# Kernel tuning notes

Measured on AMD Instinct MI355X. Metric: run time of the kernel, lower is better.

The kernel has to match this reference:

```python
import jax, jax.numpy as jnp
import numpy as np

N_NODES = 100000
N_EDGES = 1600000
NODE_F = 8   # augmented node features
EDGE_F = 2   # augmented edge features
GLOB_F = 1
HID = 16
L = 3        # message passing steps

EDGE_IN = GLOB_F + EDGE_F + 2 * NODE_F   # 19
NODE_IN = GLOB_F + EDGE_F + NODE_F       # 11
GLOB_IN = EDGE_F + NODE_F + GLOB_F       # 11


def setup_inputs() -> dict:
    key = jax.random.key(0)
    ks = jax.random.split(key, 20)
    inp = {
        "x": jax.random.normal(ks[0], (N_NODES, NODE_F), dtype=jnp.float32),
        "edge_index": jax.random.randint(ks[1], (2, N_EDGES), 0, N_NODES, dtype=jnp.int32),
        "edge_attr": jax.random.normal(ks[2], (N_EDGES, EDGE_F), dtype=jnp.float32),
        "g": jax.random.normal(ks[3], (1, GLOB_F), dtype=jnp.float32),
    }
    s = 0.1
    inp["edge_W1"] = jax.random.normal(ks[4], (L, EDGE_IN, HID), dtype=jnp.float32) * s
    inp["edge_b1"] = jnp.zeros((L, HID), dtype=jnp.float32)
    inp["edge_W2"] = jax.random.normal(ks[5], (L, HID, EDGE_F), dtype=jnp.float32) * s
    inp["edge_b2"] = jnp.zeros((L, EDGE_F), dtype=jnp.float32)
    inp["node_W1"] = jax.random.normal(ks[6], (L, NODE_IN, HID), dtype=jnp.float32) * s
    inp["node_b1"] = jnp.zeros((L, HID), dtype=jnp.float32)
    inp["node_W2"] = jax.random.normal(ks[7], (L, HID, NODE_F), dtype=jnp.float32) * s
    inp["node_b2"] = jnp.zeros((L, NODE_F), dtype=jnp.float32)
    inp["glob_W1"] = jax.random.normal(ks[8], (L, GLOB_IN, HID), dtype=jnp.float32) * s
    inp["glob_b1"] = jnp.zeros((L, HID), dtype=jnp.float32)
    inp["glob_W2"] = jax.random.normal(ks[9], (L, HID, GLOB_F), dtype=jnp.float32) * s
    inp["glob_b2"] = jnp.zeros((L, GLOB_F), dtype=jnp.float32)
    return inp


def _mlp(h, W1, b1, W2, b2):
    # two-layer MLP with ReLU after first layer only (activate_final=False, no layer_norm)
    return jnp.maximum(h @ W1 + b1, 0.0) @ W2 + b2


def reference(x, edge_index, edge_attr, g,
              edge_W1, edge_b1, edge_W2, edge_b2,
              node_W1, node_b1, node_W2, node_b2,
              glob_W1, glob_b1, glob_W2, glob_b2):
    row, col = edge_index[0], edge_index[1]
    n = x.shape[0]
    for l in range(L):
        g_e = jnp.broadcast_to(g, (row.shape[0], GLOB_F))
        # edge block: gather node features along edges, concat, MLP -> [E, EDGE_F]
        e_in = jnp.concatenate([g_e, x[row], x[col], edge_attr], axis=1)
        edge_emb = _mlp(e_in, edge_W1[l], edge_b1[l], edge_W2[l], edge_b2[l])
        # sum-aggregate edge embeddings to source nodes
        agg = jax.ops.segment_sum(edge_emb, row, num_segments=n)
        g_n = jnp.broadcast_to(g, (n, GLOB_F))
        node_emb = _mlp(jnp.concatenate([g_n, x, agg], axis=1),
                        node_W1[l], node_b1[l], node_W2[l], node_b2[l])
        # global block on mean-aggregated edge/node embeddings
        edge_gl = jnp.mean(edge_emb, axis=0, keepdims=True)
        node_gl = jnp.mean(node_emb, axis=0, keepdims=True)
        g = _mlp(jnp.concatenate([node_gl, edge_gl, g], axis=1),
                 glob_W1[l], glob_b1[l], glob_W2[l], glob_b2[l])
        x, edge_attr = node_emb, edge_emb
    return x  # final node embeddings [N, NODE_F]
```

## Files before the change

### kernel.cpp

```cpp
#include <hip/hip_runtime.h>

#define NN 100000
#define NE 1600000
#define CH 4096
#define NCHUNK ((NE + CH - 1) / CH)
#define NBUCK ((NN + 255) / 256)

__device__ __forceinline__ float wave_red(float v) {
#pragma unroll
    for (int off = 32; off > 0; off >>= 1) v += __shfl_down(v, off, 64);
    return v;
}

__global__ __launch_bounds__(256) void hist_kernel(
    const int* __restrict__ ei, int* __restrict__ hist)
{
    __shared__ int h[NBUCK];
    int t = threadIdx.x, c = blockIdx.x;
    for (int b = t; b < NBUCK; b += 256) h[b] = 0;
    __syncthreads();
    int base = c * CH;
    for (int i = t; i < CH; i += 256) {
        int e = base + i;
        if (e < NE) atomicAdd(&h[ei[e] >> 8], 1);
    }
    __syncthreads();
    for (int b = t; b < NBUCK; b += 256) hist[c * NBUCK + b] = h[b];
}

__global__ __launch_bounds__(512) void bscan_kernel(
    const int* __restrict__ hist, int* __restrict__ baseT, int* __restrict__ colTotal)
{
    __shared__ int buf[2][512];
    int b = blockIdx.x, t = threadIdx.x;
    int v = (t < NCHUNK) ? hist[t * NBUCK + b] : 0;
    buf[0][t] = v;
    __syncthreads();
    int src = 0;
    for (int d = 1; d < 512; d <<= 1) {
        int nv = buf[src][t] + ((t >= d) ? buf[src][t - d] : 0);
        buf[src ^ 1][t] = nv;
        src ^= 1;
        __syncthreads();
    }
    if (t < NCHUNK) baseT[b * NCHUNK + t] = buf[src][t] - v;
    if (t == NCHUNK - 1) colTotal[b] = buf[src][t];
}

__global__ __launch_bounds__(512) void boff_kernel(
    const int* __restrict__ colTotal, int* __restrict__ b_off)
{
    __shared__ int buf[2][512];
    int t = threadIdx.x;
    int v = (t < NBUCK) ? colTotal[t] : 0;
    buf[0][t] = v;
    __syncthreads();
    int src = 0;
    for (int d = 1; d < 512; d <<= 1) {
        int nv = buf[src][t] + ((t >= d) ? buf[src][t - d] : 0);
        buf[src ^ 1][t] = nv;
        src ^= 1;
        __syncthreads();
    }
    if (t < NBUCK) b_off[t] = buf[src][t] - v;
    if (t == NBUCK - 1) b_off[NBUCK] = buf[src][t];
}

__global__ __launch_bounds__(256) void fillb_kernel(
    const int* __restrict__ ei, const float* __restrict__ eattr,
    const int* __restrict__ baseT, const int* __restrict__ b_off,
    float4* __restrict__ rec)
{
    __shared__ int sslot[NBUCK];
    int t = threadIdx.x, c = blockIdx.x;
    for (int b = t; b < NBUCK; b += 256)
        sslot[b] = b_off[b] + baseT[b * NCHUNK + c];
    __syncthreads();
    int base = c * CH;
    for (int i = t; i < CH; i += 256) {
        int e = base + i;
        if (e < NE) {
            int row = ei[e];
            int slot = atomicAdd(&sslot[row >> 8], 1);
            float2 ea = reinterpret_cast<const float2*>(eattr)[e];
            float4 v;
            v.x = __int_as_float(row);
            v.y = __int_as_float(ei[NE + e]);
            v.z = ea.x; v.w = ea.y;
            rec[slot] = v;
        }
    }
}

__global__ __launch_bounds__(256) void prep_kernel(
    const float* __restrict__ x, const float* __restrict__ W1,
    float* __restrict__ Pr, float* __restrict__ Pc)
{
    int i = blockIdx.x * 256 + threadIdx.x;
    if (i >= NN) return;
    const float4* xi = reinterpret_cast<const float4*>(x + (size_t)i * 8);
    float4 a0 = xi[0], a1 = xi[1];
    float xv[8] = {a0.x, a0.y, a0.z, a0.w, a1.x, a1.y, a1.z, a1.w};
    float pr[16], pc[16];
#pragma unroll
    for (int q = 0; q < 16; q++) { pr[q] = 0.f; pc[q] = 0.f; }
#pragma unroll
    for (int k = 0; k < 8; k++) {
        float v = xv[k];
#pragma unroll
        for (int q = 0; q < 16; q++) {
            pr[q] += v * W1[(1 + k) * 16 + q];
            pc[q] += v * W1[(9 + k) * 16 + q];
        }
    }
    float4* po = reinterpret_cast<float4*>(Pr + (size_t)i * 16);
#pragma unroll
    for (int t = 0; t < 4; t++)
        po[t] = make_float4(pr[4 * t], pr[4 * t + 1], pr[4 * t + 2], pr[4 * t + 3]);
    float4* qo = reinterpret_cast<float4*>(Pc + (size_t)i * 16);
#pragma unroll
    for (int t = 0; t < 4; t++)
        qo[t] = make_float4(pc[4 * t], pc[4 * t + 1], pc[4 * t + 2], pc[4 * t + 3]);
}

template <bool WRITE_REC, bool NEED_SUM, bool HAS_NEXT>
__global__ __launch_bounds__(256, 4) void fused_kernel(
    float4* __restrict__ rec, const int* __restrict__ b_off,
    const float* __restrict__ PrIn, const float* __restrict__ PcIn,
    const float* __restrict__ gptr,
    const float* __restrict__ eW1, const float* __restrict__ eB1,
    const float* __restrict__ eW2, const float* __restrict__ eB2,
    const float* __restrict__ x,
    const float* __restrict__ nW1, const float* __restrict__ nB1,
    const float* __restrict__ nW2, const float* __restrict__ nB2,
    const float* __restrict__ nextW1,
    float* __restrict__ PrOut, float* __restrict__ PcOut,
    float* __restrict__ xout, float* __restrict__ sums)
{
    __shared__ float sPrT[16 * 256];
    __shared__ float sagg[256][2];
    __shared__ float redE[4][2];
    __shared__ float redN[4][8];
    int tid = threadIdx.x;
    sagg[tid][0] = 0.f; sagg[tid][1] = 0.f;

    int n0 = blockIdx.x * 256;
    int nrow = n0 + tid;
    if (nrow < NN) {
        const float4* ps = reinterpret_cast<const float4*>(PrIn + (size_t)nrow * 16);
        float4 p0 = ps[0], p1 = ps[1], p2 = ps[2], p3 = ps[3];
        sPrT[0 * 256 + tid]  = p0.x; sPrT[1 * 256 + tid]  = p0.y;
        sPrT[2 * 256 + tid]  = p0.z; sPrT[3 * 256 + tid]  = p0.w;
        sPrT[4 * 256 + tid]  = p1.x; sPrT[5 * 256 + tid]  = p1.y;
        sPrT[6 * 256 + tid]  = p1.z; sPrT[7 * 256 + tid]  = p1.w;
        sPrT[8 * 256 + tid]  = p2.x; sPrT[9 * 256 + tid]  = p2.y;
        sPrT[10 * 256 + tid] = p2.z; sPrT[11 * 256 + tid] = p2.w;
        sPrT[12 * 256 + tid] = p3.x; sPrT[13 * 256 + tid] = p3.y;
        sPrT[14 * 256 + tid] = p3.z; sPrT[15 * 256 + tid] = p3.w;
    }
    __syncthreads();

    int e0 = b_off[blockIdx.x], e1 = b_off[blockIdx.x + 1];

    float gval = gptr[0];
    float gterm[16];
#pragma unroll
    for (int q = 0; q < 16; q++) gterm[q] = eB1[q] + gval * eW1[q];

    float t0 = 0.f, t1 = 0.f;
    for (int e = e0 + tid; e < e1; e += 256) {
        float4 r = rec[e];
        int row = __float_as_int(r.x);
        int col = __float_as_int(r.y);
        float ea0 = r.z, ea1 = r.w;
        int li = row - n0;
        const float4* pc = reinterpret_cast<const float4*>(PcIn + (size_t)col * 16);
        float4 c0 = pc[0], c1 = pc[1], c2 = pc[2], c3 = pc[3];
        float h[16];
#pragma unroll
        for (int q = 0; q < 16; q++) h[q] = gterm[q] + sPrT[q * 256 + li];
        h[0]  += c0.x; h[1]  += c0.y; h[2]  += c0.z; h[3]  += c0.w;
        h[4]  += c1.x; h[5]  += c1.y; h[6]  += c1.z; h[7]  += c1.w;
        h[8]  += c2.x; h[9]  += c2.y; h[10] += c2.z; h[11] += c2.w;
        h[12] += c3.x; h[13] += c3.y; h[14] += c3.z; h[15] += c3.w;
#pragma unroll
        for (int q = 0; q < 16; q++) {
            h[q] += ea0 * eW1[17 * 16 + q];
            h[q] += ea1 * eW1[18 * 16 + q];
        }
        float s0 = eB2[0], s1 = eB2[1];
#pragma unroll
        for (int q = 0; q < 16; q++) {
            float rr = fmaxf(h[q], 0.f);
            s0 += rr * eW2[2 * q];
            s1 += rr * eW2[2 * q + 1];
        }
        if (WRITE_REC) {
            float4 w;
            w.x = r.x; w.y = r.y; w.z = s0; w.w = s1;
            rec[e] = w;
        }
        atomicAdd(&sagg[li][0], s0);
        atomicAdd(&sagg[li][1], s1);
        t0 += s0; t1 += s1;
    }

    if (NEED_SUM) {
        float r0 = wave_red(t0);
        float r1 = wave_red(t1);
        int wave = tid >> 6, lane = tid & 63;
        if (lane == 0) { redE[wave][0] = r0; redE[wave][1] = r1; }
    }
    __syncthreads();
    if (NEED_SUM && tid == 0) {
        atomicAdd(&sums[0], redE[0][0] + redE[1][0] + redE[2][0] + redE[3][0]);
        atomicAdd(&sums[1], redE[0][1] + redE[1][1] + redE[2][1] + redE[3][1]);
    }

    int n = n0 + tid;
    float out[8];
#pragma unroll
    for (int m = 0; m < 8; m++) out[m] = 0.f;

    if (n < NN) {
        float in[11];
        in[0] = gval;
        const float4* xi = reinterpret_cast<const float4*>(x + (size_t)n * 8);
        float4 a0 = xi[0], a1 = xi[1];
        in[1] = a0.x; in[2] = a0.y; in[3] = a0.z; in[4] = a0.w;
        in[5] = a1.x; in[6] = a1.y; in[7] = a1.z; in[8] = a1.w;
        in[9] = sagg[tid][0]; in[10] = sagg[tid][1];

        float h[16];
#pragma unroll
        for (int q = 0; q < 16; q++) h[q] = nB1[q];
#pragma unroll
        for (int k = 0; k < 11; k++) {
            float v = in[k];
#pragma unroll
            for (int q = 0; q < 16; q++) h[q] += v * nW1[k * 16 + q];
        }
#pragma unroll
        for (int m = 0; m < 8; m++) out[m] = nB2[m];
#pragma unroll
        for (int q = 0; q < 16; q++) {
            float hq = fmaxf(h[q], 0.f);
#pragma unroll
            for (int m = 0; m < 8; m++) out[m] += hq * nW2[q * 8 + m];
        }
        float4* xo = reinterpret_cast<float4*>(xout + (size_t)n * 8);
        xo[0] = make_float4(out[0], out[1], out[2], out[3]);
        xo[1] = make_float4(out[4], out[5], out[6], out[7]);

        if (HAS_NEXT) {
            float pr[16], pc[16];
#pragma unroll
            for (int q = 0; q < 16; q++) { pr[q] = 0.f; pc[q] = 0.f; }
#pragma unroll
            for (int k = 0; k < 8; k++) {
                float v = out[k];
#pragma unroll
                for (int q = 0; q < 16; q++) {
                    pr[q] += v * nextW1[(1 + k) * 16 + q];
                    pc[q] += v * nextW1[(9 + k) * 16 + q];
                }
            }
            float4* po = reinterpret_cast<float4*>(PrOut + (size_t)n * 16);
#pragma unroll
            for (int t = 0; t < 4; t++)
                po[t] = make_float4(pr[4*t], pr[4*t+1], pr[4*t+2], pr[4*t+3]);
            float4* qo = reinterpret_cast<float4*>(PcOut + (size_t)n * 16);
#pragma unroll
            for (int t = 0; t < 4; t++)
                qo[t] = make_float4(pc[4*t], pc[4*t+1], pc[4*t+2], pc[4*t+3]);
        }
    }
    if (NEED_SUM) {
        float r[8];
#pragma unroll
        for (int m = 0; m < 8; m++) r[m] = wave_red(out[m]);
        int wave = tid >> 6, lane = tid & 63;
        if (lane == 0) {
#pragma unroll
            for (int m = 0; m < 8; m++) redN[wave][m] = r[m];
        }
        __syncthreads();
        if (tid == 0) {
#pragma unroll
            for (int m = 0; m < 8; m++) {
                float s = redN[0][m] + redN[1][m] + redN[2][m] + redN[3][m];
                atomicAdd(&sums[2 + m], s);
            }
        }
    }
}

__global__ void glob_kernel(const float* __restrict__ sums,
                            const float* __restrict__ gold,
                            const float* __restrict__ W1, const float* __restrict__ B1,
                            const float* __restrict__ W2, const float* __restrict__ B2,
                            float* __restrict__ gnew)
{
    if (threadIdx.x == 0 && blockIdx.x == 0) {
        float in[11];
#pragma unroll
        for (int j = 0; j < 8; j++) in[j] = sums[2 + j] * (1.0f / NN);
        in[8] = sums[0] * (1.0f / NE);
        in[9] = sums[1] * (1.0f / NE);
        in[10] = gold[0];
        float acc = B2[0];
#pragma unroll
        for (int j = 0; j < 16; j++) {
            float h = B1[j];
#pragma unroll
            for (int k = 0; k < 11; k++) h += in[k] * W1[k * 16 + j];
            acc += fmaxf(h, 0.f) * W2[j];
        }
        gnew[0] = acc;
    }
}

extern "C" void kernel_launch(void* const* d_in, const int* in_sizes, int n_in,
                              void* d_out, int out_size, void* d_ws, size_t ws_size,
                              hipStream_t stream) {
    const float* x     = (const float*)d_in[0];
    const int*   ei    = (const int*)d_in[1];
    const float* eattr = (const float*)d_in[2];
    const float* g     = (const float*)d_in[3];
    const float* eW1 = (const float*)d_in[4];
    const float* eB1 = (const float*)d_in[5];
    const float* eW2 = (const float*)d_in[6];
    const float* eB2 = (const float*)d_in[7];
    const float* nW1 = (const float*)d_in[8];
    const float* nB1 = (const float*)d_in[9];
    const float* nW2 = (const float*)d_in[10];
    const float* nB2 = (const float*)d_in[11];
    const float* gW1 = (const float*)d_in[12];
    const float* gB1 = (const float*)d_in[13];
    const float* gW2 = (const float*)d_in[14];
    const float* gB2 = (const float*)d_in[15];
    float* out = (float*)d_out;

    char* ws = (char*)d_ws;
    float*  xb0    = (float*)(ws);
    int*    b_off  = (int*)  (ws + 3200000);
    float*  sums   = (float*)(ws + 3201600);
    float*  g1     = (float*)(ws + 3201728);
    float*  g2     = g1 + 1;
    float4* rec    = (float4*)(ws + 3201792);
    float*  PrA    = (float*)(ws + 28801792);
    float*  PcA    = (float*)(ws + 35201792);
    float*  PrB    = (float*)(ws + 41601792);
    float*  PcB    = (float*)(ws + 48001792);
    int*    hist     = (int*)PrB;
    int*    baseT    = (int*)((char*)PrB + 611584);
    int*    colTotal = (int*)((char*)PrB + 1223168);

    dim3 blk(256);
    dim3 cgrid(NCHUNK);
    dim3 bgrid(NBUCK);
    dim3 ngrid((NN + 255) / 256);

    hipMemsetAsync(sums, 0, 192, stream);
    hist_kernel<<<cgrid, blk, 0, stream>>>(ei, hist);
    bscan_kernel<<<bgrid, 512, 0, stream>>>(hist, baseT, colTotal);
    boff_kernel<<<1, 512, 0, stream>>>(colTotal, b_off);
    fillb_kernel<<<cgrid, blk, 0, stream>>>(ei, eattr, baseT, b_off, rec);
    prep_kernel<<<ngrid, blk, 0, stream>>>(x, eW1, PrA, PcA);

    fused_kernel<true, true, true><<<bgrid, blk, 0, stream>>>(
        rec, b_off, PrA, PcA, g,
        eW1, eB1, eW2, eB2,
        x, nW1, nB1, nW2, nB2,
        eW1 + 304, PrB, PcB, xb0, sums);
    glob_kernel<<<1, 64, 0, stream>>>(sums, g, gW1, gB1, gW2, gB2, g1);

    fused_kernel<true, true, true><<<bgrid, blk, 0, stream>>>(
        rec, b_off, PrB, PcB, g1,
        eW1 + 304, eB1 + 16, eW2 + 32, eB2 + 2,
        xb0, nW1 + 176, nB1 + 16, nW2 + 128, nB2 + 8,
        eW1 + 608, PrA, PcA, (float*)out, sums + 16);
    glob_kernel<<<1, 64, 0, stream>>>(sums + 16, g1, gW1 + 176, gB1 + 16, gW2 + 16, gB2 + 1, g2);

    fused_kernel<false, false, false><<<bgrid, blk, 0, stream>>>(
        rec, b_off, PrA, PcA, g2,
        eW1 + 608, eB1 + 32, eW2 + 64, eB2 + 4,
        (float*)out, nW1 + 352, nB1 + 32, nW2 + 256, nB2 + 16,
        nullptr, nullptr, nullptr, out, sums);
}
```

Before: 338.9 us.

## Shrink node buckets to 64 and split edge records into packed key plus attributes

Node buckets shrink from 256 to 64 nodes, so the fused kernels launch four times as many blocks. Each block also uses less shared memory and finishes with less tail imbalance. Edge records go from a 16-byte float4 to a 4-byte packed key (local row in the high bits, column in the low 17 bits) plus a separate float2 of attributes, cutting per-edge read and write traffic. In exchange, the node MLP stage runs on only 64 of 256 threads per block, and the bucket-offset scan becomes a larger single-block scan.

```diff
diff --git a/kernel.cpp b/kernel.cpp
--- a/kernel.cpp
+++ b/kernel.cpp
@@ -4,7 +4,8 @@
 #define NE 1600000
 #define CH 4096
 #define NCHUNK ((NE + CH - 1) / CH)
-#define NBUCK ((NN + 255) / 256)
+#define BUCK 64
+#define NBUCK ((NN + BUCK - 1) / BUCK)
 
 __device__ __forceinline__ float wave_red(float v) {
 #pragma unroll
@@ -22,7 +23,7 @@
     int base = c * CH;
     for (int i = t; i < CH; i += 256) {
         int e = base + i;
-        if (e < NE) atomicAdd(&h[ei[e] >> 8], 1);
+        if (e < NE) atomicAdd(&h[ei[e] >> 6], 1);
     }
     __syncthreads();
     for (int b = t; b < NBUCK; b += 256) hist[c * NBUCK + b] = h[b];
@@ -47,29 +48,33 @@
     if (t == NCHUNK - 1) colTotal[b] = buf[src][t];
 }
 
-__global__ __launch_bounds__(512) void boff_kernel(
+__global__ __launch_bounds__(1024) void boff_kernel(
     const int* __restrict__ colTotal, int* __restrict__ b_off)
 {
-    __shared__ int buf[2][512];
+    __shared__ int buf[2][2048];
     int t = threadIdx.x;
-    int v = (t < NBUCK) ? colTotal[t] : 0;
-    buf[0][t] = v;
+    for (int i = t; i < 2048; i += 1024)
+        buf[0][i] = (i < NBUCK) ? colTotal[i] : 0;
     __syncthreads();
     int src = 0;
-    for (int d = 1; d < 512; d <<= 1) {
-        int nv = buf[src][t] + ((t >= d) ? buf[src][t - d] : 0);
-        buf[src ^ 1][t] = nv;
+    for (int d = 1; d < 2048; d <<= 1) {
+        for (int i = t; i < 2048; i += 1024) {
+            int v = buf[src][i];
+            if (i >= d) v += buf[src][i - d];
+            buf[src ^ 1][i] = v;
+        }
         src ^= 1;
         __syncthreads();
     }
-    if (t < NBUCK) b_off[t] = buf[src][t] - v;
-    if (t == NBUCK - 1) b_off[NBUCK] = buf[src][t];
+    for (int i = t; i < 2048; i += 1024)
+        if (i < NBUCK) b_off[i] = buf[src][i] - colTotal[i];
+    if (t == 0) b_off[NBUCK] = buf[src][NBUCK - 1];
 }
 
 __global__ __launch_bounds__(256) void fillb_kernel(
     const int* __restrict__ ei, const float* __restrict__ eattr,
     const int* __restrict__ baseT, const int* __restrict__ b_off,
-    float4* __restrict__ rec)
+    int* __restrict__ key, float2* __restrict__ recEA)
 {
     __shared__ int sslot[NBUCK];
     int t = threadIdx.x, c = blockIdx.x;
@@ -81,13 +86,10 @@
         int e = base + i;
         if (e < NE) {
             int row = ei[e];
-            int slot = atomicAdd(&sslot[row >> 8], 1);
+            int slot = atomicAdd(&sslot[row >> 6], 1);
             float2 ea = reinterpret_cast<const float2*>(eattr)[e];
-            float4 v;
-            v.x = __int_as_float(row);
-            v.y = __int_as_float(ei[NE + e]);
-            v.z = ea.x; v.w = ea.y;
-            rec[slot] = v;
+            key[slot] = ((row & (BUCK - 1)) << 17) | ei[NE + e];
+            recEA[slot] = ea;
         }
     }
 }
@@ -125,7 +127,8 @@
 
 template <bool WRITE_REC, bool NEED_SUM, bool HAS_NEXT>
 __global__ __launch_bounds__(256, 4) void fused_kernel(
-    float4* __restrict__ rec, const int* __restrict__ b_off,
+    const int* __restrict__ key, float2* __restrict__ recEA,
+    const int* __restrict__ b_off,
     const float* __restrict__ PrIn, const float* __restrict__ PcIn,
     const float* __restrict__ gptr,
     const float* __restrict__ eW1, const float* __restrict__ eB1,
@@ -137,26 +140,24 @@
     float* __restrict__ PrOut, float* __restrict__ PcOut,
     float* __restrict__ xout, float* __restrict__ sums)
 {
-    __shared__ float sPrT[16 * 256];
-    __shared__ float sagg[256][2];
+    __shared__ float sPrT[16 * BUCK];
+    __shared__ float sagg[BUCK][2];
     __shared__ float redE[4][2];
     __shared__ float redN[4][8];
     int tid = threadIdx.x;
-    sagg[tid][0] = 0.f; sagg[tid][1] = 0.f;
-
-    int n0 = blockIdx.x * 256;
-    int nrow = n0 + tid;
-    if (nrow < NN) {
-        const float4* ps = reinterpret_cast<const float4*>(PrIn + (size_t)nrow * 16);
-        float4 p0 = ps[0], p1 = ps[1], p2 = ps[2], p3 = ps[3];
-        sPrT[0 * 256 + tid]  = p0.x; sPrT[1 * 256 + tid]  = p0.y;
-        sPrT[2 * 256 + tid]  = p0.z; sPrT[3 * 256 + tid]  = p0.w;
-        sPrT[4 * 256 + tid]  = p1.x; sPrT[5 * 256 + tid]  = p1.y;
-        sPrT[6 * 256 + tid]  = p1.z; sPrT[7 * 256 + tid]  = p1.w;
-        sPrT[8 * 256 + tid]  = p2.x; sPrT[9 * 256 + tid]  = p2.y;
-        sPrT[10 * 256 + tid] = p2.z; sPrT[11 * 256 + tid] = p2.w;
-        sPrT[12 * 256 + tid] = p3.x; sPrT[13 * 256 + tid] = p3.y;
-        sPrT[14 * 256 + tid] = p3.z; sPrT[15 * 256 + tid] = p3.w;
+    if (tid < 2 * BUCK) ((float*)sagg)[tid] = 0.f;
+
+    int n0 = blockIdx.x * BUCK;
+    {
+        int li = tid >> 2, q = tid & 3;
+        int nrow = n0 + li;
+        if (nrow < NN) {
+            float4 p = reinterpret_cast<const float4*>(PrIn + (size_t)nrow * 16)[q];
+            sPrT[(4 * q + 0) * BUCK + li] = p.x;
+            sPrT[(4 * q + 1) * BUCK + li] = p.y;
+            sPrT[(4 * q + 2) * BUCK + li] = p.z;
+            sPrT[(4 * q + 3) * BUCK + li] = p.w;
+        }
     }
     __syncthreads();
 
@@ -169,24 +170,23 @@
 
     float t0 = 0.f, t1 = 0.f;
     for (int e = e0 + tid; e < e1; e += 256) {
-        float4 r = rec[e];
-        int row = __float_as_int(r.x);
-        int col = __float_as_int(r.y);
-        float ea0 = r.z, ea1 = r.w;
-        int li = row - n0;
+        int k = key[e];
+        int col = k & 0x1FFFF;
+        int li = k >> 17;
+        float2 ea = recEA[e];
         const float4* pc = reinterpret_cast<const float4*>(PcIn + (size_t)col * 16);
         float4 c0 = pc[0], c1 = pc[1], c2 = pc[2], c3 = pc[3];
         float h[16];
 #pragma unroll
-        for (int q = 0; q < 16; q++) h[q] = gterm[q] + sPrT[q * 256 + li];
+        for (int q = 0; q < 16; q++) h[q] = gterm[q] + sPrT[q * BUCK + li];
         h[0]  += c0.x; h[1]  += c0.y; h[2]  += c0.z; h[3]  += c0.w;
         h[4]  += c1.x; h[5]  += c1.y; h[6]  += c1.z; h[7]  += c1.w;
         h[8]  += c2.x; h[9]  += c2.y; h[10] += c2.z; h[11] += c2.w;
         h[12] += c3.x; h[13] += c3.y; h[14] += c3.z; h[15] += c3.w;
 #pragma unroll
         for (int q = 0; q < 16; q++) {
-            h[q] += ea0 * eW1[17 * 16 + q];
-            h[q] += ea1 * eW1[18 * 16 + q];
+            h[q] += ea.x * eW1[17 * 16 + q];
+            h[q] += ea.y * eW1[18 * 16 + q];
         }
         float s0 = eB2[0], s1 = eB2[1];
 #pragma unroll
@@ -195,11 +195,7 @@
             s0 += rr * eW2[2 * q];
             s1 += rr * eW2[2 * q + 1];
         }
-        if (WRITE_REC) {
-            float4 w;
-            w.x = r.x; w.y = r.y; w.z = s0; w.w = s1;
-            rec[e] = w;
-        }
+        if (WRITE_REC) recEA[e] = make_float2(s0, s1);
         atomicAdd(&sagg[li][0], s0);
         atomicAdd(&sagg[li][1], s1);
         t0 += s0; t1 += s1;
@@ -222,7 +218,7 @@
 #pragma unroll
     for (int m = 0; m < 8; m++) out[m] = 0.f;
 
-    if (n < NN) {
+    if (tid < BUCK && n < NN) {
         float in[11];
         in[0] = gval;
         const float4* xi = reinterpret_cast<const float4*>(x + (size_t)n * 8);
@@ -342,48 +338,49 @@
     float* out = (float*)d_out;
 
     char* ws = (char*)d_ws;
-    float*  xb0    = (float*)(ws);
-    int*    b_off  = (int*)  (ws + 3200000);
-    float*  sums   = (float*)(ws + 3201600);
-    float*  g1     = (float*)(ws + 3201728);
-    float*  g2     = g1 + 1;
-    float4* rec    = (float4*)(ws + 3201792);
-    float*  PrA    = (float*)(ws + 28801792);
-    float*  PcA    = (float*)(ws + 35201792);
-    float*  PrB    = (float*)(ws + 41601792);
-    float*  PcB    = (float*)(ws + 48001792);
+    float*  xb0   = (float*)(ws);
+    int*    b_off = (int*)  (ws + 3200000);
+    float*  sums  = (float*)(ws + 3206400);
+    float*  g1    = (float*)(ws + 3206528);
+    float*  g2    = g1 + 1;
+    int*    key   = (int*)  (ws + 3206656);
+    float2* recEA = (float2*)(ws + 9606656);
+    float*  PrA   = (float*)(ws + 22406656);
+    float*  PcA   = (float*)(ws + 28806656);
+    float*  PrB   = (float*)(ws + 35206656);
+    float*  PcB   = (float*)(ws + 41606656);
     int*    hist     = (int*)PrB;
-    int*    baseT    = (int*)((char*)PrB + 611584);
-    int*    colTotal = (int*)((char*)PrB + 1223168);
+    int*    baseT    = (int*)((char*)PrB + 2444800);
+    int*    colTotal = (int*)((char*)PrB + 4889600);
 
     dim3 blk(256);
     dim3 cgrid(NCHUNK);
     dim3 bgrid(NBUCK);
     dim3 ngrid((NN + 255) / 256);
 
-    hipMemsetAsync(sums, 0, 192, stream);
+    hipMemsetAsync(sums, 0, 128, stream);
     hist_kernel<<<cgrid, blk, 0, stream>>>(ei, hist);
     bscan_kernel<<<bgrid, 512, 0, stream>>>(hist, baseT, colTotal);
-    boff_kernel<<<1, 512, 0, stream>>>(colTotal, b_off);
-    fillb_kernel<<<cgrid, blk, 0, stream>>>(ei, eattr, baseT, b_off, rec);
+    boff_kernel<<<1, 1024, 0, stream>>>(colTotal, b_off);
+    fillb_kernel<<<cgrid, blk, 0, stream>>>(ei, eattr, baseT, b_off, key, recEA);
     prep_kernel<<<ngrid, blk, 0, stream>>>(x, eW1, PrA, PcA);
 
     fused_kernel<true, true, true><<<bgrid, blk, 0, stream>>>(
-        rec, b_off, PrA, PcA, g,
+        key, recEA, b_off, PrA, PcA, g,
         eW1, eB1, eW2, eB2,
         x, nW1, nB1, nW2, nB2,
         eW1 + 304, PrB, PcB, xb0, sums);
     glob_kernel<<<1, 64, 0, stream>>>(sums, g, gW1, gB1, gW2, gB2, g1);
 
     fused_kernel<true, true, true><<<bgrid, blk, 0, stream>>>(
-        rec, b_off, PrB, PcB, g1,
+        key, recEA, b_off, PrB, PcB, g1,
         eW1 + 304, eB1 + 16, eW2 + 32, eB2 + 2,
         xb0, nW1 + 176, nB1 + 16, nW2 + 128, nB2 + 8,
         eW1 + 608, PrA, PcA, (float*)out, sums + 16);
     glob_kernel<<<1, 64, 0, stream>>>(sums + 16, g1, gW1 + 176, gB1 + 16, gW2 + 16, gB2 + 1, g2);
 
     fused_kernel<false, false, false><<<bgrid, blk, 0, stream>>>(
-        rec, b_off, PrA, PcA, g2,
+        key, recEA, b_off, PrA, PcA, g2,
         eW1 + 608, eB1 + 32, eW2 + 64, eB2 + 4,
         (float*)out, nW1 + 352, nB1 + 32, nW2 + 256, nB2 + 16,
         nullptr, nullptr, nullptr, out, sums);
```

After: 645.3 us. 90.4% more time.

## Recompute per-edge column projection from raw node features instead of precomputed tables

Applied to the files above, without the earlier changes.

Removes the precomputed per-node projections (Pr/Pc, 16 floats each) and the prep kernel. Each edge now gathers the 8-float column node feature and multiplies it by the 8x16 weight block inline, and each block computes its row projection into shared memory from x. This halves the bytes fetched per random column gather and drops the 128 B/node projection writes, at the cost of about 128 extra FMAs per edge. Workspace buffers are reorganized, and a second node buffer replaces the projection buffers.

```diff
diff --git a/kernel.cpp b/kernel.cpp
--- a/kernel.cpp
+++ b/kernel.cpp
@@ -92,49 +92,15 @@
     }
 }
 
-__global__ __launch_bounds__(256) void prep_kernel(
-    const float* __restrict__ x, const float* __restrict__ W1,
-    float* __restrict__ Pr, float* __restrict__ Pc)
-{
-    int i = blockIdx.x * 256 + threadIdx.x;
-    if (i >= NN) return;
-    const float4* xi = reinterpret_cast<const float4*>(x + (size_t)i * 8);
-    float4 a0 = xi[0], a1 = xi[1];
-    float xv[8] = {a0.x, a0.y, a0.z, a0.w, a1.x, a1.y, a1.z, a1.w};
-    float pr[16], pc[16];
-#pragma unroll
-    for (int q = 0; q < 16; q++) { pr[q] = 0.f; pc[q] = 0.f; }
-#pragma unroll
-    for (int k = 0; k < 8; k++) {
-        float v = xv[k];
-#pragma unroll
-        for (int q = 0; q < 16; q++) {
-            pr[q] += v * W1[(1 + k) * 16 + q];
-            pc[q] += v * W1[(9 + k) * 16 + q];
-        }
-    }
-    float4* po = reinterpret_cast<float4*>(Pr + (size_t)i * 16);
-#pragma unroll
-    for (int t = 0; t < 4; t++)
-        po[t] = make_float4(pr[4 * t], pr[4 * t + 1], pr[4 * t + 2], pr[4 * t + 3]);
-    float4* qo = reinterpret_cast<float4*>(Pc + (size_t)i * 16);
-#pragma unroll
-    for (int t = 0; t < 4; t++)
-        qo[t] = make_float4(pc[4 * t], pc[4 * t + 1], pc[4 * t + 2], pc[4 * t + 3]);
-}
-
-template <bool WRITE_REC, bool NEED_SUM, bool HAS_NEXT>
+template <bool WRITE_REC, bool NEED_SUM>
 __global__ __launch_bounds__(256, 4) void fused_kernel(
     float4* __restrict__ rec, const int* __restrict__ b_off,
-    const float* __restrict__ PrIn, const float* __restrict__ PcIn,
     const float* __restrict__ gptr,
     const float* __restrict__ eW1, const float* __restrict__ eB1,
     const float* __restrict__ eW2, const float* __restrict__ eB2,
-    const float* __restrict__ x,
+    const float* __restrict__ xin,
     const float* __restrict__ nW1, const float* __restrict__ nB1,
     const float* __restrict__ nW2, const float* __restrict__ nB2,
-    const float* __restrict__ nextW1,
-    float* __restrict__ PrOut, float* __restrict__ PcOut,
     float* __restrict__ xout, float* __restrict__ sums)
 {
     __shared__ float sPrT[16 * 256];
@@ -147,16 +113,20 @@
     int n0 = blockIdx.x * 256;
     int nrow = n0 + tid;
     if (nrow < NN) {
-        const float4* ps = reinterpret_cast<const float4*>(PrIn + (size_t)nrow * 16);
-        float4 p0 = ps[0], p1 = ps[1], p2 = ps[2], p3 = ps[3];
-        sPrT[0 * 256 + tid]  = p0.x; sPrT[1 * 256 + tid]  = p0.y;
-        sPrT[2 * 256 + tid]  = p0.z; sPrT[3 * 256 + tid]  = p0.w;
-        sPrT[4 * 256 + tid]  = p1.x; sPrT[5 * 256 + tid]  = p1.y;
-        sPrT[6 * 256 + tid]  = p1.z; sPrT[7 * 256 + tid]  = p1.w;
-        sPrT[8 * 256 + tid]  = p2.x; sPrT[9 * 256 + tid]  = p2.y;
-        sPrT[10 * 256 + tid] = p2.z; sPrT[11 * 256 + tid] = p2.w;
-        sPrT[12 * 256 + tid] = p3.x; sPrT[13 * 256 + tid] = p3.y;
-        sPrT[14 * 256 + tid] = p3.z; sPrT[15 * 256 + tid] = p3.w;
+        const float4* xi = reinterpret_cast<const float4*>(xin + (size_t)nrow * 8);
+        float4 a0 = xi[0], a1 = xi[1];
+        float xv[8] = {a0.x, a0.y, a0.z, a0.w, a1.x, a1.y, a1.z, a1.w};
+        float pr[16];
+#pragma unroll
+        for (int q = 0; q < 16; q++) pr[q] = 0.f;
+#pragma unroll
+        for (int k = 0; k < 8; k++) {
+            float v = xv[k];
+#pragma unroll
+            for (int q = 0; q < 16; q++) pr[q] += v * eW1[(1 + k) * 16 + q];
+        }
+#pragma unroll
+        for (int q = 0; q < 16; q++) sPrT[q * 256 + tid] = pr[q];
     }
     __syncthreads();
 
@@ -174,15 +144,18 @@
         int col = __float_as_int(r.y);
         float ea0 = r.z, ea1 = r.w;
         int li = row - n0;
-        const float4* pc = reinterpret_cast<const float4*>(PcIn + (size_t)col * 16);
-        float4 c0 = pc[0], c1 = pc[1], c2 = pc[2], c3 = pc[3];
+        const float4* xc4 = reinterpret_cast<const float4*>(xin + (size_t)col * 8);
+        float4 c0 = xc4[0], c1 = xc4[1];
+        float xc[8] = {c0.x, c0.y, c0.z, c0.w, c1.x, c1.y, c1.z, c1.w};
         float h[16];
 #pragma unroll
         for (int q = 0; q < 16; q++) h[q] = gterm[q] + sPrT[q * 256 + li];
-        h[0]  += c0.x; h[1]  += c0.y; h[2]  += c0.z; h[3]  += c0.w;
-        h[4]  += c1.x; h[5]  += c1.y; h[6]  += c1.z; h[7]  += c1.w;
-        h[8]  += c2.x; h[9]  += c2.y; h[10] += c2.z; h[11] += c2.w;
-        h[12] += c3.x; h[13] += c3.y; h[14] += c3.z; h[15] += c3.w;
+#pragma unroll
+        for (int k = 0; k < 8; k++) {
+            float v = xc[k];
+#pragma unroll
+            for (int q = 0; q < 16; q++) h[q] += v * eW1[(9 + k) * 16 + q];
+        }
 #pragma unroll
         for (int q = 0; q < 16; q++) {
             h[q] += ea0 * eW1[17 * 16 + q];
@@ -225,7 +198,7 @@
     if (n < NN) {
         float in[11];
         in[0] = gval;
-        const float4* xi = reinterpret_cast<const float4*>(x + (size_t)n * 8);
+        const float4* xi = reinterpret_cast<const float4*>(xin + (size_t)n * 8);
         float4 a0 = xi[0], a1 = xi[1];
         in[1] = a0.x; in[2] = a0.y; in[3] = a0.z; in[4] = a0.w;
         in[5] = a1.x; in[6] = a1.y; in[7] = a1.z; in[8] = a1.w;
@@ -251,29 +224,6 @@
         float4* xo = reinterpret_cast<float4*>(xout + (size_t)n * 8);
         xo[0] = make_float4(out[0], out[1], out[2], out[3]);
         xo[1] = make_float4(out[4], out[5], out[6], out[7]);
-
-        if (HAS_NEXT) {
-            float pr[16], pc[16];
-#pragma unroll
-            for (int q = 0; q < 16; q++) { pr[q] = 0.f; pc[q] = 0.f; }
-#pragma unroll
-            for (int k = 0; k < 8; k++) {
-                float v = out[k];
-#pragma unroll
-                for (int q = 0; q < 16; q++) {
-                    pr[q] += v * nextW1[(1 + k) * 16 + q];
-                    pc[q] += v * nextW1[(9 + k) * 16 + q];
-                }
-            }
-            float4* po = reinterpret_cast<float4*>(PrOut + (size_t)n * 16);
-#pragma unroll
-            for (int t = 0; t < 4; t++)
-                po[t] = make_float4(pr[4*t], pr[4*t+1], pr[4*t+2], pr[4*t+3]);
-            float4* qo = reinterpret_cast<float4*>(PcOut + (size_t)n * 16);
-#pragma unroll
-            for (int t = 0; t < 4; t++)
-                qo[t] = make_float4(pc[4*t], pc[4*t+1], pc[4*t+2], pc[4*t+3]);
-        }
     }
     if (NEED_SUM) {
         float r[8];
@@ -342,49 +292,45 @@
     float* out = (float*)d_out;
 
     char* ws = (char*)d_ws;
-    float*  xb0    = (float*)(ws);
-    int*    b_off  = (int*)  (ws + 3200000);
-    float*  sums   = (float*)(ws + 3201600);
-    float*  g1     = (float*)(ws + 3201728);
-    float*  g2     = g1 + 1;
-    float4* rec    = (float4*)(ws + 3201792);
-    float*  PrA    = (float*)(ws + 28801792);
-    float*  PcA    = (float*)(ws + 35201792);
-    float*  PrB    = (float*)(ws + 41601792);
-    float*  PcB    = (float*)(ws + 48001792);
-    int*    hist     = (int*)PrB;
-    int*    baseT    = (int*)((char*)PrB + 611584);
-    int*    colTotal = (int*)((char*)PrB + 1223168);
+    float*  xb0   = (float*)(ws);
+    float*  xb1   = (float*)(ws + 3200000);
+    int*    b_off = (int*)  (ws + 6400000);
+    float*  sums  = (float*)(ws + 6401600);
+    float*  g1    = (float*)(ws + 6401728);
+    float*  g2    = g1 + 1;
+    float4* rec   = (float4*)(ws + 6401792);
+    int*    hist     = (int*)xb1;
+    int*    baseT    = (int*)((char*)xb1 + 611584);
+    int*    colTotal = (int*)((char*)xb1 + 1223168);
 
     dim3 blk(256);
     dim3 cgrid(NCHUNK);
     dim3 bgrid(NBUCK);
     dim3 ngrid((NN + 255) / 256);
 
-    hipMemsetAsync(sums, 0, 192, stream);
+    hipMemsetAsync(sums, 0, 128, stream);
     hist_kernel<<<cgrid, blk, 0, stream>>>(ei, hist);
     bscan_kernel<<<bgrid, 512, 0, stream>>>(hist, baseT, colTotal);
     boff_kernel<<<1, 512, 0, stream>>>(colTotal, b_off);
     fillb_kernel<<<cgrid, blk, 0, stream>>>(ei, eattr, baseT, b_off, rec);
-    prep_kernel<<<ngrid, blk, 0, stream>>>(x, eW1, PrA, PcA);
-
-    fused_kernel<true, true, true><<<bgrid, blk, 0, stream>>>(
-        rec, b_off, PrA, PcA, g,
+
+    fused_kernel<true, true><<<bgrid, blk, 0, stream>>>(
+        rec, b_off, g,
         eW1, eB1, eW2, eB2,
         x, nW1, nB1, nW2, nB2,
-        eW1 + 304, PrB, PcB, xb0, sums);
+        xb0, sums);
     glob_kernel<<<1, 64, 0, stream>>>(sums, g, gW1, gB1, gW2, gB2, g1);
 
-    fused_kernel<true, true, true><<<bgrid, blk, 0, stream>>>(
-        rec, b_off, PrB, PcB, g1,
+    fused_kernel<true, true><<<bgrid, blk, 0, stream>>>(
+        rec, b_off, g1,
         eW1 + 304, eB1 + 16, eW2 + 32, eB2 + 2,
         xb0, nW1 + 176, nB1 + 16, nW2 + 128, nB2 + 8,
-        eW1 + 608, PrA, PcA, (float*)out, sums + 16);
+        xb1, sums + 16);
     glob_kernel<<<1, 64, 0, stream>>>(sums + 16, g1, gW1 + 176, gB1 + 16, gW2 + 16, gB2 + 1, g2);
 
-    fused_kernel<false, false, false><<<bgrid, blk, 0, stream>>>(
-        rec, b_off, PrA, PcA, g2,
+    fused_kernel<false, false><<<bgrid, blk, 0, stream>>>(
+        rec, b_off, g2,
         eW1 + 608, eB1 + 32, eW2 + 64, eB2 + 4,
-        (float*)out, nW1 + 352, nB1 + 32, nW2 + 256, nB2 + 16,
-        nullptr, nullptr, nullptr, out, sums);
-}
+        xb1, nW1 + 352, nB1 + 32, nW2 + 256, nB2 + 16,
+        out, sums);
+}
```

New measurement: 354.9 us. +4.7%, slower.
